# Kernel tuning notes

Hardware: AMD Instinct MI355X
Metric: run time of the kernel (lower is better)

The kernel has to match this reference:

```python
import jax, jax.numpy as jnp
import numpy as np

H, KVH, D = 8, 4, 256
SCALING = 256.0 ** -0.5   # query_pre_attn_scalar ** -0.5
SOFTCAP = 50.0
THETA = 10000.0
WINDOW = 1024


def setup_inputs() -> dict:
    key = jax.random.key(0)
    ks = jax.random.split(key, 5)
    B, S, HID = 2, 2048, 2304
    return {
        "hidden_states": jax.random.normal(ks[0], (B, S, HID), jnp.float32),
        "Wq": jax.random.normal(ks[1], (H * D, HID), jnp.float32) * 0.02,
        "Wk": jax.random.normal(ks[2], (KVH * D, HID), jnp.float32) * 0.02,
        "Wv": jax.random.normal(ks[3], (KVH * D, HID), jnp.float32) * 0.02,
        "Wo": jax.random.normal(ks[4], (HID, H * D), jnp.float32) * 0.02,
        "position_ids": jnp.arange(S, dtype=jnp.int32),
    }


def _rotate_half(x):
    x1, x2 = x[..., : D // 2], x[..., D // 2 :]
    return jnp.concatenate((-x2, x1), axis=-1)


def reference(hidden_states, Wq, Wk, Wv, Wo, position_ids):
    B, S, HID = hidden_states.shape
    # projections (torch Linear: y = x @ W.T)
    q = (hidden_states @ Wq.T).reshape(B, S, H, D).transpose(0, 2, 1, 3)      # [B,H,S,D]
    k = (hidden_states @ Wk.T).reshape(B, S, KVH, D).transpose(0, 2, 1, 3)    # [B,KVH,S,D]
    v = (hidden_states @ Wv.T).reshape(B, S, KVH, D).transpose(0, 2, 1, 3)

    # rotary embedding
    inv_freq = 1.0 / (THETA ** (jnp.arange(0, D, 2, dtype=jnp.float32) / D))  # [D/2]
    freqs = position_ids.astype(jnp.float32)[:, None] * inv_freq[None, :]     # [S,D/2]
    emb = jnp.concatenate((freqs, freqs), axis=-1)                            # [S,D]
    cos = jnp.cos(emb)[None, None]                                            # [1,1,S,D]
    sin = jnp.sin(emb)[None, None]
    q = q * cos + _rotate_half(q) * sin
    k = k * cos + _rotate_half(k) * sin

    # repeat_kv (GQA)
    n_rep = H // KVH
    k = jnp.repeat(k, n_rep, axis=1)  # [B,H,S,D]
    v = jnp.repeat(v, n_rep, axis=1)

    # softcapped attention scores
    scores = jnp.einsum("bhqd,bhkd->bhqk", q, k) * SCALING
    scores = SOFTCAP * jnp.tanh(scores / SOFTCAP)

    # causal + sliding-window mask
    i = jnp.arange(S)[:, None]
    j = jnp.arange(S)[None, :]
    allowed = (j <= i) & (i - j < WINDOW)
    scores = jnp.where(allowed[None, None], scores, jnp.finfo(scores.dtype).min)

    attn = jax.nn.softmax(scores.astype(jnp.float32), axis=-1).astype(q.dtype)
    out = jnp.einsum("bhqk,bhkd->bhqd", attn, v)          # [B,H,S,D]
    out = out.transpose(0, 2, 1, 3).reshape(B, S, H * D)   # [B,S,H*D]
    return out @ Wo.T                                      # [B,S,HID]
```

## Files before the change

### kernel.cpp

```cpp
#include <hip/hip_runtime.h>

typedef _Float16 half8 __attribute__((ext_vector_type(8)));
typedef _Float16 half4v __attribute__((ext_vector_type(4)));
typedef float floatx4 __attribute__((ext_vector_type(4)));

#define GLD16(g, l) __builtin_amdgcn_global_load_lds(                          \
    (__attribute__((address_space(1))) void*)(g),                              \
    (__attribute__((address_space(3))) void*)(l), 16, 0, 0)

#define VM4 asm volatile("s_waitcnt vmcnt(4)" ::: "memory")
#define VM0 asm volatile("s_waitcnt vmcnt(0)" ::: "memory")

__global__ void cvt_all(const float* __restrict__ s0, const float* __restrict__ s1,
                        const float* __restrict__ s2, const float* __restrict__ s3,
                        const float* __restrict__ s4, _Float16* __restrict__ d0,
                        _Float16* __restrict__ d1, _Float16* __restrict__ d2,
                        _Float16* __restrict__ d3, _Float16* __restrict__ d4) {
  long i = (long)blockIdx.x * 256 + threadIdx.x;
  const float* s;
  _Float16* d;
  long off;
  if (i < 2359296) { s = s0; d = d0; off = i; }
  else if (i < 3538944) { s = s1; d = d1; off = i - 2359296; }
  else if (i < 4128768) { s = s2; d = d2; off = i - 3538944; }
  else if (i < 4718592) { s = s3; d = d3; off = i - 4128768; }
  else { s = s4; d = d4; off = i - 4718592; }
  const float4 v = *(const float4*)(s + off * 4);
  half4v o = {(_Float16)v.x, (_Float16)v.y, (_Float16)v.z, (_Float16)v.w};
  *(half4v*)(d + off * 4) = o;
}

__device__ __forceinline__ void stg_half(const _Float16* __restrict__ g,
                                         _Float16* l, int h, long k0, int K,
                                         int tid, const long* gofs) {
#pragma unroll
  for (int p = 0; p < 2; ++p)
    GLD16(g + (long)h * 128 * K + k0 + gofs[p],
          l + (h * 1024 + p * 512 + tid) * 8);
}

#define LDB(buf)                                                               \
  _Pragma("unroll") for (int n = 0; n < 4; ++n)                                \
  _Pragma("unroll") for (int ks = 0; ks < 2; ++ks)                             \
      bfr[n][ks] = *(const half8*)&lB[buf][boff0 + n * 1024 +                  \
                                           (((ks * 4 + quad) ^ xq) << 3)];

#define PH(buf, q, VMW, ...)                                                   \
  {                                                                            \
    half8 af[2][2];                                                            \
    _Pragma("unroll") for (int m2 = 0; m2 < 2; ++m2)                           \
    _Pragma("unroll") for (int ks = 0; ks < 2; ++ks)                           \
        af[m2][ks] = *(const half8*)&lA[buf][aoff0 + ((q) * 2 + m2) * 1024 +   \
                                             (((ks * 4 + quad) ^ xq) << 3)];   \
    __VA_ARGS__;                                                               \
    __builtin_amdgcn_sched_barrier(0);                                         \
    __builtin_amdgcn_s_barrier();                                              \
    __builtin_amdgcn_sched_barrier(0);                                         \
    __builtin_amdgcn_s_setprio(1);                                             \
    _Pragma("unroll") for (int ks = 0; ks < 2; ++ks)                           \
    _Pragma("unroll") for (int m2 = 0; m2 < 2; ++m2)                           \
    _Pragma("unroll") for (int n = 0; n < 4; ++n)                              \
        acc[(q) * 2 + m2][n] = __builtin_amdgcn_mfma_f32_16x16x32_f16(         \
            af[m2][ks], bfr[n][ks], acc[(q) * 2 + m2][n], 0, 0, 0);            \
    __builtin_amdgcn_s_setprio(0);                                             \
    VMW;                                                                       \
    __builtin_amdgcn_sched_barrier(0);                                         \
    __builtin_amdgcn_s_barrier();                                              \
    __builtin_amdgcn_sched_barrier(0);                                         \
  }

template <typename TO>
__global__ __launch_bounds__(512, 2) void gemm256(
    const _Float16* __restrict__ A, const _Float16* __restrict__ B,
    TO* __restrict__ C, int M, int N, int K) {
  __shared__ __align__(16) _Float16 lA[2][16384];
  __shared__ __align__(16) _Float16 lB[2][16384];
  const int tid = threadIdx.x;
  const int lane = tid & 63;
  const int w = tid >> 6;
  const int wm = w >> 2, wn = w & 3;
  const int quad = lane >> 4, l15 = lane & 15;
  const int xq = l15 & 7;

  const int nwg = gridDim.x * gridDim.y;
  int wg = blockIdx.y * gridDim.x + blockIdx.x;
  if (!(nwg & 7)) wg = (wg & 7) * (nwg >> 3) + (wg >> 3);
  const int bx = wg % gridDim.x, by = wg / gridDim.x;
  const long tM = (long)by * 256, tN = (long)bx * 256;

  const _Float16* Ab = A + tM * K;
  const _Float16* Bb = B + tN * K;

  long gofs[2];
#pragma unroll
  for (int p = 0; p < 2; ++p) {
    const int U = p * 512 + tid;
    const int r = U >> 3;
    gofs[p] = (long)r * K + (((U & 7) ^ (r & 7)) << 3);
  }

  const int aoff0 = (wm * 128 + l15) * 64;
  const int boff0 = (wn * 64 + l15) * 64;

  floatx4 acc[8][4] = {};
  half8 bfr[4][2];

  stg_half(Bb, &lB[0][0], 0, 0, K, tid, gofs);
  stg_half(Bb, &lB[0][0], 1, 0, K, tid, gofs);
  stg_half(Ab, &lA[0][0], 0, 0, K, tid, gofs);
  stg_half(Ab, &lA[0][0], 1, 0, K, tid, gofs);
  stg_half(Bb, &lB[1][0], 0, 64, K, tid, gofs);
  stg_half(Bb, &lB[1][0], 1, 64, K, tid, gofs);
  VM4;
  __builtin_amdgcn_sched_barrier(0);
  __builtin_amdgcn_s_barrier();
  __builtin_amdgcn_sched_barrier(0);

  const int NI = K >> 7;
  for (int i = 0; i < NI; ++i) {
    const long ks0 = (long)i << 7;
    const bool fin = (i == NI - 1);
    LDB(0);
    PH(0, 0, (void)0, stg_half(Ab, &lA[1][0], 0, ks0 + 64, K, tid, gofs));
    PH(0, 1, (void)0, stg_half(Ab, &lA[1][0], 1, ks0 + 64, K, tid, gofs));
    PH(0, 2, (void)0,
       if (!fin) stg_half(Bb, &lB[0][0], 0, ks0 + 128, K, tid, gofs));
    PH(0, 3, if (fin) { VM0; } else { VM4; },
       if (!fin) stg_half(Bb, &lB[0][0], 1, ks0 + 128, K, tid, gofs));
    LDB(1);
    PH(1, 0, (void)0,
       if (!fin) stg_half(Ab, &lA[0][0], 0, ks0 + 128, K, tid, gofs));
    PH(1, 1, (void)0,
       if (!fin) stg_half(Ab, &lA[0][0], 1, ks0 + 128, K, tid, gofs));
    PH(1, 2, (void)0,
       if (!fin) stg_half(Bb, &lB[1][0], 0, ks0 + 192, K, tid, gofs));
    PH(1, 3, if (!fin) { VM4; },
       if (!fin) stg_half(Bb, &lB[1][0], 1, ks0 + 192, K, tid, gofs));
  }

#pragma unroll
  for (int m = 0; m < 8; ++m) {
#pragma unroll
    for (int n = 0; n < 4; ++n) {
      const long col = tN + wn * 64 + n * 16 + l15;
      const long row0 = tM + wm * 128 + m * 16 + quad * 4;
#pragma unroll
      for (int r = 0; r < 4; ++r)
        C[(row0 + r) * N + col] = (TO)acc[m][n][r];
    }
  }
}

__global__ void rope_qk(const _Float16* __restrict__ QKV,
                        const int* __restrict__ pos_ids,
                        _Float16* __restrict__ Qr, _Float16* __restrict__ Kr) {
  const int idx = blockIdx.x * blockDim.x + threadIdx.x;
  const int d = idx & 127;
  const int rest = idx >> 7;
  const int head = rest % 12;
  const int ms = rest / 12;
  const int s = ms & 2047;
  const int b = ms >> 11;
  const float ang = (float)pos_ids[s] * expf(d * -0.07195578164f);
  const float c = cosf(ang), sn = sinf(ang);
  if (head < 8) {
    const _Float16* src = QKV + (long)ms * 4096 + head * 256 + d;
    const float x1 = (float)src[0], x2 = (float)src[128];
    _Float16* dst = Qr + (((long)b * 8 + head) * 2048 + s) * 256 + d;
    dst[0] = (_Float16)(x1 * c - x2 * sn);
    dst[128] = (_Float16)(x2 * c + x1 * sn);
  } else {
    const int kh = head - 8;
    const _Float16* src = QKV + (long)ms * 4096 + 2048 + kh * 256 + d;
    const float x1 = (float)src[0], x2 = (float)src[128];
    _Float16* dst = Kr + (((long)b * 4 + kh) * 2048 + s) * 256 + d;
    dst[0] = (_Float16)(x1 * c - x2 * sn);
    dst[128] = (_Float16)(x2 * c + x1 * sn);
  }
}

__global__ void vtrans(const _Float16* __restrict__ QKV,
                       _Float16* __restrict__ Vt) {
  __shared__ _Float16 lT[64 * 65];
  const int tid = threadIdx.x;
  const int ss = blockIdx.x * 64;
  const int dd = blockIdx.y * 64;
  const int z = blockIdx.z;
  const int b = z >> 2, kvh = z & 3;

#pragma unroll
  for (int pass = 0; pass < 2; ++pass) {
    const int U = pass * 256 + tid;
    const int s_loc = U >> 3, du = U & 7;
    const half8 v = *(const half8*)(QKV + ((long)(b * 2048 + ss + s_loc)) * 4096 +
                                    3072 + kvh * 256 + dd + du * 8);
#pragma unroll
    for (int e = 0; e < 8; ++e) lT[s_loc * 65 + du * 8 + e] = v[e];
  }
  __syncthreads();
#pragma unroll
  for (int pass = 0; pass < 2; ++pass) {
    const int U = pass * 256 + tid;
    const int su = U & 7, dl = (U >> 3) & 63;
    half8 o;
#pragma unroll
    for (int e = 0; e < 8; ++e) o[e] = lT[(su * 8 + e) * 65 + dl];
    *(half8*)(Vt + ((long)z * 256 + dd + dl) * 2048 + ss + su * 8) = o;
  }
}

__global__ __launch_bounds__(256, 2) void attn_fwd(
    const _Float16* __restrict__ Q, const _Float16* __restrict__ K,
    const _Float16* __restrict__ Vt, _Float16* __restrict__ AO) {
  __shared__ __align__(16) _Float16 lK[2][64 * 256];
  __shared__ __align__(16) _Float16 lP[64 * 76];

  const int tid = threadIdx.x;
  const int lane = tid & 63;
  const int w = tid >> 6;
  const int quad = lane >> 4, l15 = lane & 15;

  const int qt = blockIdx.x;
  const int h = blockIdx.y;
  const int b = blockIdx.z;
  const int kvh = h >> 1;
  const int qs = qt * 64;

  const _Float16* Qb = Q + (((long)b * 8 + h) * 2048) * 256;
  const _Float16* Kb = K + (((long)b * 4 + kvh) * 2048) * 256;
  const _Float16* Vb = Vt + (((long)b * 4 + kvh) * 256) * 2048;

  half8 qf[8];
  {
    const _Float16* qp = Qb + (long)(qs + w * 16 + l15) * 256 + quad * 8;
#pragma unroll
    for (int t = 0; t < 8; ++t) qf[t] = *(const half8*)(qp + t * 32);
  }
  half8 onesv;
#pragma unroll
  for (int e = 0; e < 8; ++e) onesv[e] = (_Float16)1.f;

  floatx4 o[4][4] = {};
  floatx4 lacc[4] = {};

  const int kt_lo = qt >= 16 ? qt - 16 : 0;

  {
    const _Float16* kt0 = Kb + (long)kt_lo * 64 * 256;
#pragma unroll
    for (int p = 0; p < 8; ++p) {
      const int U = p * 256 + tid;
      const int r = U >> 5, u = U & 31;
      GLD16(kt0 + r * 256 + ((u ^ (r & 7)) << 3), &lK[0][U * 8]);
    }
  }

  int cur = 0;
  for (int kt = kt_lo; kt <= qt; ++kt, cur ^= 1) {
    const int ks = kt * 64;
    __syncthreads();

    half8 vf[2][4];
#pragma unroll
    for (int t2 = 0; t2 < 2; ++t2)
#pragma unroll
      for (int j = 0; j < 4; ++j) {
        const int d = w * 64 + j * 16 + l15;
        vf[t2][j] = *(const half8*)(Vb + (long)d * 2048 + ks + t2 * 32 + quad * 8);
      }
    if (kt < qt) {
      const _Float16* kt0 = Kb + (long)(ks + 64) * 256;
      const int nxt = cur ^ 1;
#pragma unroll
      for (int p = 0; p < 8; ++p) {
        const int U = p * 256 + tid;
        const int r = U >> 5, u = U & 31;
        GLD16(kt0 + r * 256 + ((u ^ (r & 7)) << 3), &lK[nxt][U * 8]);
      }
    }

    floatx4 sc[4] = {};
#pragma unroll
    for (int t = 0; t < 8; ++t)
#pragma unroll
      for (int j = 0; j < 4; ++j) {
        const half8 kf = *(const half8*)&lK[cur][(j * 16 + l15) * 256 +
                                                 (((t * 4 + quad) ^ (l15 & 7)) << 3)];
        sc[j] = __builtin_amdgcn_mfma_f32_16x16x32_f16(qf[t], kf, sc[j], 0, 0, 0);
      }

    const bool need_mask = (kt == qt) || (kt == qt - 16);
    const int qr0 = qs + w * 16 + quad * 4;
#pragma unroll
    for (int j = 0; j < 4; ++j) {
      const int key = ks + j * 16 + l15;
#pragma unroll
      for (int r = 0; r < 4; ++r) {
        const float s = sc[j][r] * 0.0625f;
        const float t2 = (s * 0.02f) * (s * 0.02f);
        const float cap = s * (1.f + t2 * (-0.33333333f + t2 * 0.13333333f));
        float p = __expf(cap - 5.f);
        if (need_mask) {
          const bool ok = (key <= qr0 + r) && (qr0 + r - key < 1024);
          p = ok ? p : 0.f;
        }
        lP[(w * 16 + quad * 4 + r) * 76 + j * 16 + l15] = (_Float16)p;
      }
    }
    __syncthreads();

#pragma unroll
    for (int t2 = 0; t2 < 2; ++t2) {
      half8 pf[4];
#pragma unroll
      for (int i = 0; i < 4; ++i)
        pf[i] = *(const half8*)&lP[(i * 16 + l15) * 76 + t2 * 32 + quad * 8];
#pragma unroll
      for (int i = 0; i < 4; ++i) {
        lacc[i] = __builtin_amdgcn_mfma_f32_16x16x32_f16(pf[i], onesv, lacc[i],
                                                         0, 0, 0);
#pragma unroll
        for (int j = 0; j < 4; ++j)
          o[i][j] = __builtin_amdgcn_mfma_f32_16x16x32_f16(pf[i], vf[t2][j],
                                                           o[i][j], 0, 0, 0);
      }
    }
  }

  _Float16* aop = AO + ((long)b * 2048 + qs) * 2048 + (long)h * 256;
#pragma unroll
  for (int i = 0; i < 4; ++i)
#pragma unroll
    for (int r = 0; r < 4; ++r) {
      const int row = i * 16 + quad * 4 + r;
      const float inv = 1.0f / lacc[i][r];
#pragma unroll
      for (int j = 0; j < 4; ++j)
        aop[(long)row * 2048 + w * 64 + j * 16 + l15] =
            (_Float16)(o[i][j][r] * inv);
    }
}

extern "C" void kernel_launch(void* const* d_in, const int* in_sizes, int n_in,
                              void* d_out, int out_size, void* d_ws,
                              size_t ws_size, hipStream_t stream) {
  const float* hs = (const float*)d_in[0];
  const float* Wq = (const float*)d_in[1];
  const float* Wk = (const float*)d_in[2];
  const float* Wv = (const float*)d_in[3];
  const float* Wo = (const float*)d_in[4];
  const int* pos = (const int*)d_in[5];
  float* out = (float*)d_out;

  _Float16* Xf = (_Float16*)d_ws;
  _Float16* Wqkv = Xf + 4096L * 2304;
  _Float16* Wo16 = Wqkv + 4096L * 2304;
  _Float16* QKV = Wo16 + 2304L * 2048;
  _Float16* Qr = QKV + 4096L * 4096;
  _Float16* Kr = Qr + 2L * 8 * 2048 * 256;
  _Float16* Vt = Kr + 2L * 4 * 2048 * 256;
  _Float16* AO = Xf;

  cvt_all<<<dim3(23040), dim3(256), 0, stream>>>(
      hs, Wq, Wk, Wv, Wo, Xf, Wqkv, Wqkv + 2048L * 2304, Wqkv + 3072L * 2304,
      Wo16);

  gemm256<_Float16><<<dim3(16, 16), dim3(512), 0, stream>>>(Xf, Wqkv, QKV,
                                                            4096, 4096, 2304);
  rope_qk<<<dim3(2 * 2048 * 12 * 128 / 256), dim3(256), 0, stream>>>(QKV, pos,
                                                                     Qr, Kr);
  vtrans<<<dim3(32, 4, 8), dim3(256), 0, stream>>>(QKV, Vt);
  attn_fwd<<<dim3(32, 8, 2), dim3(256), 0, stream>>>(Qr, Kr, Vt, AO);
  gemm256<float><<<dim3(9, 16), dim3(512), 0, stream>>>(AO, Wo16, out, 4096,
                                                        2304, 2048);
}
```

Before: 358.8 us.

## Restructure GEMM main loop with register double-buffered A fragments and fewer barriers

The fp16 GEMM loop is rescheduled so that A fragments for the next phase are read from LDS into a second register set while the current phase's MFMAs run. The loop now uses one barrier per phase instead of two, and stages whole A and B k-tiles at once with a full vmcnt(0) wait. The goal is to cut barrier stalls and hide LDS read latency, at the cost of more registers and a shallower global-load overlap. The RoPE kernel also switches to fast __expf/__cosf/__sinf intrinsics, which may lose accuracy for large angles.

```diff
diff --git a/kernel.cpp b/kernel.cpp
--- a/kernel.cpp
+++ b/kernel.cpp
@@ -8,7 +8,6 @@
     (__attribute__((address_space(1))) void*)(g),                              \
     (__attribute__((address_space(3))) void*)(l), 16, 0, 0)
 
-#define VM4 asm volatile("s_waitcnt vmcnt(4)" ::: "memory")
 #define VM0 asm volatile("s_waitcnt vmcnt(0)" ::: "memory")
 
 __global__ void cvt_all(const float* __restrict__ s0, const float* __restrict__ s1,
@@ -39,35 +38,31 @@
           l + (h * 1024 + p * 512 + tid) * 8);
 }
 
+#define BAR                                                                    \
+  __builtin_amdgcn_sched_barrier(0);                                           \
+  __builtin_amdgcn_s_barrier();                                                \
+  __builtin_amdgcn_sched_barrier(0)
+
 #define LDB(buf)                                                               \
   _Pragma("unroll") for (int n = 0; n < 4; ++n)                                \
   _Pragma("unroll") for (int ks = 0; ks < 2; ++ks)                             \
       bfr[n][ks] = *(const half8*)&lB[buf][boff0 + n * 1024 +                  \
                                            (((ks * 4 + quad) ^ xq) << 3)];
 
-#define PH(buf, q, VMW, ...)                                                   \
-  {                                                                            \
-    half8 af[2][2];                                                            \
-    _Pragma("unroll") for (int m2 = 0; m2 < 2; ++m2)                           \
-    _Pragma("unroll") for (int ks = 0; ks < 2; ++ks)                           \
-        af[m2][ks] = *(const half8*)&lA[buf][aoff0 + ((q) * 2 + m2) * 1024 +   \
-                                             (((ks * 4 + quad) ^ xq) << 3)];   \
-    __VA_ARGS__;                                                               \
-    __builtin_amdgcn_sched_barrier(0);                                         \
-    __builtin_amdgcn_s_barrier();                                              \
-    __builtin_amdgcn_sched_barrier(0);                                         \
-    __builtin_amdgcn_s_setprio(1);                                             \
-    _Pragma("unroll") for (int ks = 0; ks < 2; ++ks)                           \
-    _Pragma("unroll") for (int m2 = 0; m2 < 2; ++m2)                           \
-    _Pragma("unroll") for (int n = 0; n < 4; ++n)                              \
-        acc[(q) * 2 + m2][n] = __builtin_amdgcn_mfma_f32_16x16x32_f16(         \
-            af[m2][ks], bfr[n][ks], acc[(q) * 2 + m2][n], 0, 0, 0);            \
-    __builtin_amdgcn_s_setprio(0);                                             \
-    VMW;                                                                       \
-    __builtin_amdgcn_sched_barrier(0);                                         \
-    __builtin_amdgcn_s_barrier();                                              \
-    __builtin_amdgcn_sched_barrier(0);                                         \
-  }
+#define READA(DST, buf, q)                                                     \
+  _Pragma("unroll") for (int m2 = 0; m2 < 2; ++m2)                             \
+  _Pragma("unroll") for (int ks = 0; ks < 2; ++ks)                             \
+      DST[m2][ks] = *(const half8*)&lA[buf][aoff0 + ((q) * 2 + m2) * 1024 +    \
+                                            (((ks * 4 + quad) ^ xq) << 3)];
+
+#define MFMA16(AF, q)                                                          \
+  __builtin_amdgcn_s_setprio(1);                                               \
+  _Pragma("unroll") for (int ks = 0; ks < 2; ++ks)                             \
+  _Pragma("unroll") for (int m2 = 0; m2 < 2; ++m2)                             \
+  _Pragma("unroll") for (int n = 0; n < 4; ++n)                                \
+      acc[(q) * 2 + m2][n] = __builtin_amdgcn_mfma_f32_16x16x32_f16(           \
+          AF[m2][ks], bfr[n][ks], acc[(q) * 2 + m2][n], 0, 0, 0);              \
+  __builtin_amdgcn_s_setprio(0)
 
 template <typename TO>
 __global__ __launch_bounds__(512, 2) void gemm256(
@@ -104,38 +99,62 @@
 
   floatx4 acc[8][4] = {};
   half8 bfr[4][2];
-
+  half8 afA[2][2], afB[2][2];
+
+  stg_half(Ab, &lA[0][0], 0, 0, K, tid, gofs);
+  stg_half(Ab, &lA[0][0], 1, 0, K, tid, gofs);
   stg_half(Bb, &lB[0][0], 0, 0, K, tid, gofs);
   stg_half(Bb, &lB[0][0], 1, 0, K, tid, gofs);
-  stg_half(Ab, &lA[0][0], 0, 0, K, tid, gofs);
-  stg_half(Ab, &lA[0][0], 1, 0, K, tid, gofs);
-  stg_half(Bb, &lB[1][0], 0, 64, K, tid, gofs);
-  stg_half(Bb, &lB[1][0], 1, 64, K, tid, gofs);
-  VM4;
-  __builtin_amdgcn_sched_barrier(0);
-  __builtin_amdgcn_s_barrier();
-  __builtin_amdgcn_sched_barrier(0);
+  VM0;
+  BAR;
+  LDB(0);
+  READA(afA, 0, 0);
 
   const int NI = K >> 7;
   for (int i = 0; i < NI; ++i) {
-    const long ks0 = (long)i << 7;
+    const long k1 = ((long)i << 7) + 64;
+    const long k2 = k1 + 64;
     const bool fin = (i == NI - 1);
-    LDB(0);
-    PH(0, 0, (void)0, stg_half(Ab, &lA[1][0], 0, ks0 + 64, K, tid, gofs));
-    PH(0, 1, (void)0, stg_half(Ab, &lA[1][0], 1, ks0 + 64, K, tid, gofs));
-    PH(0, 2, (void)0,
-       if (!fin) stg_half(Bb, &lB[0][0], 0, ks0 + 128, K, tid, gofs));
-    PH(0, 3, if (fin) { VM0; } else { VM4; },
-       if (!fin) stg_half(Bb, &lB[0][0], 1, ks0 + 128, K, tid, gofs));
+    BAR;
+    stg_half(Ab, &lA[1][0], 0, k1, K, tid, gofs);
+    stg_half(Ab, &lA[1][0], 1, k1, K, tid, gofs);
+    stg_half(Bb, &lB[1][0], 0, k1, K, tid, gofs);
+    stg_half(Bb, &lB[1][0], 1, k1, K, tid, gofs);
+    READA(afB, 0, 1);
+    MFMA16(afA, 0);
+    BAR;
+    READA(afA, 0, 2);
+    MFMA16(afB, 1);
+    BAR;
+    READA(afB, 0, 3);
+    MFMA16(afA, 2);
+    VM0;
+    BAR;
+    MFMA16(afB, 3);
     LDB(1);
-    PH(1, 0, (void)0,
-       if (!fin) stg_half(Ab, &lA[0][0], 0, ks0 + 128, K, tid, gofs));
-    PH(1, 1, (void)0,
-       if (!fin) stg_half(Ab, &lA[0][0], 1, ks0 + 128, K, tid, gofs));
-    PH(1, 2, (void)0,
-       if (!fin) stg_half(Bb, &lB[1][0], 0, ks0 + 192, K, tid, gofs));
-    PH(1, 3, if (!fin) { VM4; },
-       if (!fin) stg_half(Bb, &lB[1][0], 1, ks0 + 192, K, tid, gofs));
+    READA(afA, 1, 0);
+    BAR;
+    if (!fin) {
+      stg_half(Ab, &lA[0][0], 0, k2, K, tid, gofs);
+      stg_half(Ab, &lA[0][0], 1, k2, K, tid, gofs);
+      stg_half(Bb, &lB[0][0], 0, k2, K, tid, gofs);
+      stg_half(Bb, &lB[0][0], 1, k2, K, tid, gofs);
+    }
+    READA(afB, 1, 1);
+    MFMA16(afA, 0);
+    BAR;
+    READA(afA, 1, 2);
+    MFMA16(afB, 1);
+    BAR;
+    READA(afB, 1, 3);
+    MFMA16(afA, 2);
+    if (!fin) VM0;
+    BAR;
+    MFMA16(afB, 3);
+    if (!fin) {
+      LDB(0);
+      READA(afA, 0, 0);
+    }
   }
 
 #pragma unroll
@@ -161,8 +180,8 @@
   const int ms = rest / 12;
   const int s = ms & 2047;
   const int b = ms >> 11;
-  const float ang = (float)pos_ids[s] * expf(d * -0.07195578164f);
-  const float c = cosf(ang), sn = sinf(ang);
+  const float ang = (float)pos_ids[s] * __expf(d * -0.07195578164f);
+  const float c = __cosf(ang), sn = __sinf(ang);
   if (head < 8) {
     const _Float16* src = QKV + (long)ms * 4096 + head * 256 + d;
     const float x1 = (float)src[0], x2 = (float)src[128];
```

After: 361.8 us. About the same (+0.8%).

## Fuse RoPE into QKV projection GEMM epilogue via interleaved weight rows

Applied to the files above, without the earlier changes.

Rows of Wq and Wk are permuted during fp16 conversion so that each rotary pair (d, d+128) lands in adjacent output columns. The QKV GEMM epilogue then applies the rotary rotation with a lane shuffle and writes Q and K directly into the head-major Qr/Kr buffers. This removes the separate rope_qk kernel and its extra read and write of the Q/K portion of QKV. In exchange the epilogue does scattered 2-byte stores and computes sincos per element, and the permuted row gather in cvt_all adds index math.

```diff
diff --git a/kernel.cpp b/kernel.cpp
--- a/kernel.cpp
+++ b/kernel.cpp
@@ -3,6 +3,7 @@
 typedef _Float16 half8 __attribute__((ext_vector_type(8)));
 typedef _Float16 half4v __attribute__((ext_vector_type(4)));
 typedef float floatx4 __attribute__((ext_vector_type(4)));
+typedef float floatx16 __attribute__((ext_vector_type(16)));
 
 #define GLD16(g, l) __builtin_amdgcn_global_load_lds(                          \
     (__attribute__((address_space(1))) void*)(g),                              \
@@ -20,12 +21,27 @@
   const float* s;
   _Float16* d;
   long off;
-  if (i < 2359296) { s = s0; d = d0; off = i; }
-  else if (i < 3538944) { s = s1; d = d1; off = i - 2359296; }
-  else if (i < 4128768) { s = s2; d = d2; off = i - 3538944; }
-  else if (i < 4718592) { s = s3; d = d3; off = i - 4128768; }
-  else { s = s4; d = d4; off = i - 4718592; }
-  const float4 v = *(const float4*)(s + off * 4);
+  long roff;
+  if (i < 2359296) {
+    s = s0; d = d0; off = i; roff = off;
+  } else if (i < 3538944) {
+    s = s1; d = d1; off = i - 2359296;
+    const int r = (int)(off / 576), cu = (int)(off % 576);
+    const int h = r >> 8, e = r & 255;
+    const int srcr = (h << 8) + ((e & 1) ? (e >> 1) + 128 : (e >> 1));
+    roff = (long)srcr * 576 + cu;
+  } else if (i < 4128768) {
+    s = s2; d = d2; off = i - 3538944;
+    const int r = (int)(off / 576), cu = (int)(off % 576);
+    const int h = r >> 8, e = r & 255;
+    const int srcr = (h << 8) + ((e & 1) ? (e >> 1) + 128 : (e >> 1));
+    roff = (long)srcr * 576 + cu;
+  } else if (i < 4718592) {
+    s = s3; d = d3; off = i - 4128768; roff = off;
+  } else {
+    s = s4; d = d4; off = i - 4718592; roff = off;
+  }
+  const float4 v = *(const float4*)(s + roff * 4);
   half4v o = {(_Float16)v.x, (_Float16)v.y, (_Float16)v.z, (_Float16)v.w};
   *(half4v*)(d + off * 4) = o;
 }
@@ -69,10 +85,11 @@
     __builtin_amdgcn_sched_barrier(0);                                         \
   }
 
-template <typename TO>
+template <typename TO, bool ROPE>
 __global__ __launch_bounds__(512, 2) void gemm256(
     const _Float16* __restrict__ A, const _Float16* __restrict__ B,
-    TO* __restrict__ C, int M, int N, int K) {
+    TO* __restrict__ C, int M, int N, int K, _Float16* __restrict__ Qr,
+    _Float16* __restrict__ Kr, const int* __restrict__ pos) {
   __shared__ __align__(16) _Float16 lA[2][16384];
   __shared__ __align__(16) _Float16 lB[2][16384];
   const int tid = threadIdx.x;
@@ -138,6 +155,45 @@
        if (!fin) stg_half(Bb, &lB[1][0], 1, ks0 + 192, K, tid, gofs));
   }
 
+  if constexpr (ROPE) {
+    if (tN < 3072) {
+      const int b = (int)(tM >> 11);
+      const int s0 = (int)(tM & 2047);
+      _Float16* dst0;
+      if (tN < 2048)
+        dst0 = Qr + (((long)b * 8 + (int)(tN >> 8)) * 2048) * 256;
+      else
+        dst0 = Kr + (((long)b * 4 + (int)((tN - 2048) >> 8)) * 2048) * 256;
+      const int par = l15 & 1;
+      float invf[4];
+      int dofs[4];
+#pragma unroll
+      for (int n = 0; n < 4; ++n) {
+        const int p = wn * 32 + n * 8 + (l15 >> 1);
+        invf[n] = __expf((float)p * -0.07195578164f);
+        dofs[n] = p + par * 128;
+      }
+#pragma unroll
+      for (int m = 0; m < 8; ++m) {
+#pragma unroll
+        for (int r = 0; r < 4; ++r) {
+          const int row = wm * 128 + m * 16 + quad * 4 + r;
+          const float pv = (float)pos[s0 + row];
+          _Float16* drow = dst0 + ((long)(s0 + row)) * 256;
+#pragma unroll
+          for (int n = 0; n < 4; ++n) {
+            const float v = acc[m][n][r];
+            const float px = __shfl_xor(v, 1, 64);
+            float sn, cs;
+            __sincosf(pv * invf[n], &sn, &cs);
+            const float o = par ? (v * cs + px * sn) : (v * cs - px * sn);
+            drow[dofs[n]] = (_Float16)o;
+          }
+        }
+      }
+      return;
+    }
+  }
 #pragma unroll
   for (int m = 0; m < 8; ++m) {
 #pragma unroll
@@ -148,34 +204,6 @@
       for (int r = 0; r < 4; ++r)
         C[(row0 + r) * N + col] = (TO)acc[m][n][r];
     }
-  }
-}
-
-__global__ void rope_qk(const _Float16* __restrict__ QKV,
-                        const int* __restrict__ pos_ids,
-                        _Float16* __restrict__ Qr, _Float16* __restrict__ Kr) {
-  const int idx = blockIdx.x * blockDim.x + threadIdx.x;
-  const int d = idx & 127;
-  const int rest = idx >> 7;
-  const int head = rest % 12;
-  const int ms = rest / 12;
-  const int s = ms & 2047;
-  const int b = ms >> 11;
-  const float ang = (float)pos_ids[s] * expf(d * -0.07195578164f);
-  const float c = cosf(ang), sn = sinf(ang);
-  if (head < 8) {
-    const _Float16* src = QKV + (long)ms * 4096 + head * 256 + d;
-    const float x1 = (float)src[0], x2 = (float)src[128];
-    _Float16* dst = Qr + (((long)b * 8 + head) * 2048 + s) * 256 + d;
-    dst[0] = (_Float16)(x1 * c - x2 * sn);
-    dst[128] = (_Float16)(x2 * c + x1 * sn);
-  } else {
-    const int kh = head - 8;
-    const _Float16* src = QKV + (long)ms * 4096 + 2048 + kh * 256 + d;
-    const float x1 = (float)src[0], x2 = (float)src[128];
-    _Float16* dst = Kr + (((long)b * 4 + kh) * 2048 + s) * 256 + d;
-    dst[0] = (_Float16)(x1 * c - x2 * sn);
-    dst[128] = (_Float16)(x2 * c + x1 * sn);
   }
 }
 
@@ -365,12 +393,10 @@
       hs, Wq, Wk, Wv, Wo, Xf, Wqkv, Wqkv + 2048L * 2304, Wqkv + 3072L * 2304,
       Wo16);
 
-  gemm256<_Float16><<<dim3(16, 16), dim3(512), 0, stream>>>(Xf, Wqkv, QKV,
-                                                            4096, 4096, 2304);
-  rope_qk<<<dim3(2 * 2048 * 12 * 128 / 256), dim3(256), 0, stream>>>(QKV, pos,
-                                                                     Qr, Kr);
+  gemm256<_Float16, true><<<dim3(16, 16), dim3(512), 0, stream>>>(
+      Xf, Wqkv, QKV, 4096, 4096, 2304, Qr, Kr, pos);
   vtrans<<<dim3(32, 4, 8), dim3(256), 0, stream>>>(QKV, Vt);
   attn_fwd<<<dim3(32, 8, 2), dim3(256), 0, stream>>>(Qr, Kr, Vt, AO);
-  gemm256<float><<<dim3(9, 16), dim3(512), 0, stream>>>(AO, Wo16, out, 4096,
-                                                        2304, 2048);
-}
+  gemm256<float, false><<<dim3(9, 16), dim3(512), 0, stream>>>(
+      AO, Wo16, out, 4096, 2304, 2048, nullptr, nullptr, nullptr);
+}
```

Result: faster. 331.8 us (-7.5%).
